# Kernel tuning notes

Measured on AMD Instinct MI355X. Metric: run time of the kernel, lower is better.

Reference implementation:

```python
import jax, jax.numpy as jnp
from jax import lax
import numpy as np

THRESHOLD = 0.8
SECONDARY = 0.6
SECONDARY_WEIGHT = 0.5
BN_EPS = 1e-5


def _conv_relu_pool(x, W, b):
    # x: [B,C,H,W], W: [O,I,3,3]
    y = lax.conv_general_dilated(x, W, window_strides=(1, 1), padding='SAME',
                                 dimension_numbers=('NCHW', 'OIHW', 'NCHW'))
    y = y + b[None, :, None, None]
    y = jax.nn.relu(y)
    return lax.reduce_window(y, -jnp.inf, lax.max, (1, 1, 2, 2), (1, 1, 2, 2), 'VALID')


def setup_inputs() -> dict:
    key = jax.random.key(0)
    ks = jax.random.split(key, 12)
    B, H, W = 1024, 64, 64
    d0, d1, d2 = 4096, 1024, 256  # qnn_arch
    inp = {}
    inp['x'] = jax.random.normal(ks[0], (B, 1, H, W), dtype=jnp.float32)
    # conv params (kaiming-ish scaling)
    inp['cw1'] = jax.random.normal(ks[1], (8, 1, 3, 3), jnp.float32) * (1.0 / np.sqrt(1 * 9))
    inp['cb1'] = jax.random.normal(ks[2], (8,), jnp.float32) * 0.01
    inp['cw2'] = jax.random.normal(ks[3], (16, 8, 3, 3), jnp.float32) * (1.0 / np.sqrt(8 * 9))
    inp['cb2'] = jax.random.normal(ks[4], (16,), jnp.float32) * 0.01
    # linear layers of the 'graph QNN'
    inp['w1'] = jax.random.normal(ks[5], (d1, d0), jnp.float32) * (1.0 / np.sqrt(d0))
    inp['b1'] = jax.random.normal(ks[6], (d1,), jnp.float32) * 0.01
    inp['w2'] = jax.random.normal(ks[7], (d2, d1), jnp.float32) * (1.0 / np.sqrt(d1))
    inp['b2'] = jax.random.normal(ks[8], (d2,), jnp.float32) * 0.01
    # BatchNorm1d affine params
    inp['gamma'] = jnp.ones((d2,), jnp.float32)
    inp['beta'] = jnp.zeros((d2,), jnp.float32)
    return inp


def reference(x, cw1, cb1, cw2, cb2, w1, b1, w2, b2, gamma, beta):
    B = x.shape[0]
    # CNN feature extractor
    feat = _conv_relu_pool(x, cw1, cb1)
    feat = _conv_relu_pool(feat, cw2, cb2)
    flat = feat.reshape(B, -1)                      # [B, 4096]
    # graph-QNN layers with tanh
    h1 = jnp.tanh(flat @ w1.T + b1)                 # [B, 1024]
    last = jnp.tanh(h1 @ w2.T + b2)                 # [B, 256]
    # fidelity adjacency: vectorized normalize + Gram + squared cosine
    norms = jnp.linalg.norm(last, axis=1, keepdims=True)  # [B,1]
    nrm = last / (norms + 1e-12)
    fid = (nrm @ nrm.T) ** 2                        # [B, B]
    adj = jnp.where(fid >= THRESHOLD, 1.0,
                    jnp.where(fid >= SECONDARY, SECONDARY_WEIGHT, 0.0))
    adj = adj * (1.0 - jnp.eye(B, dtype=adj.dtype))  # no self-edges
    # BatchNorm1d (training mode: batch statistics, biased variance)
    mean = jnp.mean(last, axis=0)
    var = jnp.mean((last - mean) ** 2, axis=0)
    out = (last - mean) / jnp.sqrt(var + BN_EPS) * gamma + beta
    return out, adj
```

## Files before the change

kernel.cpp:

```cpp
#include <hip/hip_runtime.h>
#include <hip/hip_bf16.h>
#include <math.h>


__global__ __launch_bounds__(256) void conv1_kernel(
    const float* __restrict__ x, const float* __restrict__ cw1,
    const float* __restrict__ cb1, float* __restrict__ feat1) {
  __shared__ float sX[66 * 66];
  __shared__ float sW1[72];
  __shared__ float sB1[8];

  const int b = blockIdx.x;
  const int t = threadIdx.x;

  for (int i = t; i < 66 * 66; i += 256) sX[i] = 0.0f;
  if (t < 72) sW1[t] = cw1[t];
  if (t < 8)  sB1[t] = cb1[t];
  __syncthreads();

  const float* xb = x + (size_t)b * 4096;
  for (int i = t; i < 4096; i += 256)
    sX[((i >> 6) + 1) * 66 + (i & 63) + 1] = xb[i];
  __syncthreads();

  for (int task = t; task < 2048; task += 256) {
    const int ch = task >> 8;
    const int rem = task & 255;
    const int py = rem >> 3;
    const int px0 = (rem & 7) * 4;

    double w9[9];
#pragma unroll
    for (int k = 0; k < 9; ++k) w9[k] = (double)sW1[ch * 9 + k];

    float reg[4][10];
#pragma unroll
    for (int r = 0; r < 4; ++r)
#pragma unroll
      for (int c = 0; c < 5; ++c) {
        const float2 v =
            *(const float2*)&sX[(2 * py + r) * 66 + 2 * px0 + 2 * c];
        reg[r][2 * c] = v.x;
        reg[r][2 * c + 1] = v.y;
      }

    float out4[4];
#pragma unroll
    for (int px = 0; px < 4; ++px) {
      double best = -1e300;
#pragma unroll
      for (int dy = 0; dy < 2; ++dy) {
#pragma unroll
        for (int dx = 0; dx < 2; ++dx) {
          double s = 0.0;
#pragma unroll
          for (int ky = 0; ky < 3; ++ky)
#pragma unroll
            for (int kx = 0; kx < 3; ++kx)
              s = fma((double)reg[dy + ky][2 * px + dx + kx], w9[ky * 3 + kx],
                      s);
          best = fmax(best, s);
        }
      }
      out4[px] = (float)fmax(best + (double)sB1[ch], 0.0);
    }
    *(float4*)&feat1[(size_t)b * 8192 + ch * 1024 + py * 32 + px0] =
        make_float4(out4[0], out4[1], out4[2], out4[3]);
  }
}

__global__ __launch_bounds__(256) void conv2_kernel(
    const float* __restrict__ feat1, const float* __restrict__ cw2,
    const float* __restrict__ cb2, float* __restrict__ flat) {
  __shared__ float sF[8 * 34 * 34];
  __shared__ float sW2[1152];
  __shared__ float sB2[16];

  const int b = blockIdx.x;
  const int t = threadIdx.x;

  for (int i = t; i < 8 * 34 * 34; i += 256) sF[i] = 0.0f;
  for (int i = t; i < 1152; i += 256) sW2[i] = cw2[i];
  if (t < 16) sB2[t] = cb2[t];
  __syncthreads();

  const float* fb = feat1 + (size_t)b * 8192;
  for (int i = t; i < 8192; i += 256) {
    const int ch = i >> 10, pos = i & 1023;
    sF[ch * 1156 + ((pos >> 5) + 1) * 34 + (pos & 31) + 1] = fb[i];
  }
  __syncthreads();

  const int py = t >> 4, px = t & 15;
  float* ob = flat + (size_t)b * 4096 + py * 16 + px;

#pragma unroll 1
  for (int oh = 0; oh < 2; ++oh) {
    double acc[8][4];
#pragma unroll
    for (int o = 0; o < 8; ++o)
#pragma unroll
      for (int q = 0; q < 4; ++q) acc[o][q] = 0.0;

#pragma unroll
    for (int ic = 0; ic < 8; ++ic) {
      float r[4][4];
#pragma unroll
      for (int iy = 0; iy < 4; ++iy) {
        const float2 v0 =
            *(const float2*)&sF[ic * 1156 + (2 * py + iy) * 34 + 2 * px];
        const float2 v1 =
            *(const float2*)&sF[ic * 1156 + (2 * py + iy) * 34 + 2 * px + 2];
        r[iy][0] = v0.x; r[iy][1] = v0.y; r[iy][2] = v1.x; r[iy][3] = v1.y;
      }
#pragma unroll
      for (int o = 0; o < 8; ++o) {
        const float* w = &sW2[(oh * 8 + o) * 72 + ic * 9];
        double w9[9];
#pragma unroll
        for (int k = 0; k < 9; ++k) w9[k] = (double)w[k];
#pragma unroll
        for (int dy = 0; dy < 2; ++dy)
#pragma unroll
          for (int dx = 0; dx < 2; ++dx) {
            double s = acc[o][dy * 2 + dx];
#pragma unroll
            for (int ky = 0; ky < 3; ++ky)
#pragma unroll
              for (int kx = 0; kx < 3; ++kx)
                s = fma((double)r[dy + ky][dx + kx], w9[ky * 3 + kx], s);
            acc[o][dy * 2 + dx] = s;
          }
      }
    }
#pragma unroll
    for (int o = 0; o < 8; ++o) {
      const int oc = oh * 8 + o;
      const double best =
          fmax(fmax(acc[o][0], acc[o][1]), fmax(acc[o][2], acc[o][3]));
      ob[oc * 256] = (float)fmax(best + (double)sB2[oc], 0.0);
    }
  }
}

__global__ __launch_bounds__(256) void conv_fused(
    const float* __restrict__ x,
    const float* __restrict__ cw1, const float* __restrict__ cb1,
    const float* __restrict__ cw2, const float* __restrict__ cb2,
    float* __restrict__ flat) {
  __shared__ float sX[66 * 66];
  __shared__ float sF[8 * 34 * 34];
  __shared__ float sW1[72];
  __shared__ float sW2[1152];
  __shared__ float sB1[8];
  __shared__ float sB2[16];

  const int b = blockIdx.x;
  const int t = threadIdx.x;

  for (int i = t; i < 66 * 66; i += 256) sX[i] = 0.0f;
  for (int i = t; i < 8 * 34 * 34; i += 256) sF[i] = 0.0f;
  if (t < 72) sW1[t] = cw1[t];
  for (int i = t; i < 1152; i += 256) sW2[i] = cw2[i];
  if (t < 8)  sB1[t] = cb1[t];
  if (t < 16) sB2[t] = cb2[t];
  __syncthreads();

  const float* xb = x + (size_t)b * 4096;
  for (int i = t; i < 4096; i += 256)
    sX[((i >> 6) + 1) * 66 + (i & 63) + 1] = xb[i];
  __syncthreads();

  for (int p = t; p < 8192; p += 256) {
    const int ch = p >> 10, pos = p & 1023;
    const int py1 = pos >> 5, px1 = pos & 31;
    double best = -1e300;
#pragma unroll
    for (int dy = 0; dy < 2; ++dy)
#pragma unroll
      for (int dx = 0; dx < 2; ++dx) {
        const int y = 2 * py1 + dy, xx = 2 * px1 + dx;
        double s = 0.0;
#pragma unroll
        for (int ky = 0; ky < 3; ++ky)
#pragma unroll
          for (int kx = 0; kx < 3; ++kx)
            s = fma((double)sX[(y + ky) * 66 + xx + kx],
                    (double)sW1[ch * 9 + ky * 3 + kx], s);
        best = fmax(best, s);
      }
    sF[ch * 1156 + (py1 + 1) * 34 + px1 + 1] =
        (float)fmax(best + (double)sB1[ch], 0.0);
  }
  __syncthreads();

  const int py = t >> 4, px = t & 15;
  for (int oh = 0; oh < 2; ++oh) {
    double acc[8][4];
#pragma unroll
    for (int o = 0; o < 8; ++o)
#pragma unroll
      for (int q = 0; q < 4; ++q) acc[o][q] = 0.0;
#pragma unroll
    for (int ic = 0; ic < 8; ++ic) {
      double r[4][4];
#pragma unroll
      for (int iy = 0; iy < 4; ++iy)
#pragma unroll
        for (int ix = 0; ix < 4; ++ix)
          r[iy][ix] = (double)sF[ic * 1156 + (2 * py + iy) * 34 + 2 * px + ix];
#pragma unroll
      for (int o = 0; o < 8; ++o) {
        const float* w = &sW2[(oh * 8 + o) * 72 + ic * 9];
        double w9[9];
#pragma unroll
        for (int k = 0; k < 9; ++k) w9[k] = (double)w[k];
#pragma unroll
        for (int dy = 0; dy < 2; ++dy)
#pragma unroll
          for (int dx = 0; dx < 2; ++dx) {
            double s = acc[o][dy * 2 + dx];
#pragma unroll
            for (int ky = 0; ky < 3; ++ky)
#pragma unroll
              for (int kx = 0; kx < 3; ++kx)
                s = fma(r[dy + ky][dx + kx], w9[ky * 3 + kx], s);
            acc[o][dy * 2 + dx] = s;
          }
      }
    }
    float* ob = flat + (size_t)b * 4096 + py * 16 + px;
#pragma unroll
    for (int o = 0; o < 8; ++o) {
      const int oc = oh * 8 + o;
      double best =
          fmax(fmax(acc[o][0], acc[o][1]), fmax(acc[o][2], acc[o][3]));
      ob[oc * 256] = (float)fmax(best + (double)sB2[oc], 0.0);
    }
  }
}

__global__ __launch_bounds__(256) void gemm_nt_f64_v3(
    const float* __restrict__ A, const float* __restrict__ B,
    double* __restrict__ P, int M, int N, int K, int Kc) {
  __shared__ double As[16][130];
  __shared__ double Bs[16][130];

  const int t = threadIdx.x;
  const int n0 = blockIdx.x * 128;
  const int m0 = blockIdx.y * 128;
  const int s  = blockIdx.z;
  const int kb = s * Kc;
  const int rS = t >> 2;
  const int cS = (t & 3) * 4;
  const int ty = t >> 4;
  const int tx = t & 15;

  double acc[8][8];
#pragma unroll
  for (int i = 0; i < 8; ++i)
#pragma unroll
    for (int j = 0; j < 8; ++j) acc[i][j] = 0.0;

  const float* Alo = &A[(size_t)(m0 + rS) * K + cS];
  const float* Ahi = &A[(size_t)(m0 + 64 + rS) * K + cS];
  const float* Blo = &B[(size_t)(n0 + rS) * K + cS];
  const float* Bhi = &B[(size_t)(n0 + 64 + rS) * K + cS];

  float4 a0 = *(const float4*)&Alo[kb];
  float4 a1 = *(const float4*)&Ahi[kb];
  float4 b0 = *(const float4*)&Blo[kb];
  float4 b1 = *(const float4*)&Bhi[kb];

  for (int k0 = kb; k0 < kb + Kc; k0 += 16) {
    __syncthreads();
    As[cS + 0][rS] = (double)a0.x; As[cS + 1][rS] = (double)a0.y;
    As[cS + 2][rS] = (double)a0.z; As[cS + 3][rS] = (double)a0.w;
    As[cS + 0][64 + rS] = (double)a1.x; As[cS + 1][64 + rS] = (double)a1.y;
    As[cS + 2][64 + rS] = (double)a1.z; As[cS + 3][64 + rS] = (double)a1.w;
    Bs[cS + 0][rS] = (double)b0.x; Bs[cS + 1][rS] = (double)b0.y;
    Bs[cS + 2][rS] = (double)b0.z; Bs[cS + 3][rS] = (double)b0.w;
    Bs[cS + 0][64 + rS] = (double)b1.x; Bs[cS + 1][64 + rS] = (double)b1.y;
    Bs[cS + 2][64 + rS] = (double)b1.z; Bs[cS + 3][64 + rS] = (double)b1.w;
    if (k0 + 16 < kb + Kc) {
      a0 = *(const float4*)&Alo[k0 + 16];
      a1 = *(const float4*)&Ahi[k0 + 16];
      b0 = *(const float4*)&Blo[k0 + 16];
      b1 = *(const float4*)&Bhi[k0 + 16];
    }
    __syncthreads();
#pragma unroll
    for (int k = 0; k < 16; ++k) {
      double ar[8], br[8];
#pragma unroll
      for (int g = 0; g < 4; ++g) {
        const double2 av = *(const double2*)&As[k][32 * g + 2 * ty];
        ar[2 * g] = av.x; ar[2 * g + 1] = av.y;
        const double2 bv = *(const double2*)&Bs[k][32 * g + 2 * tx];
        br[2 * g] = bv.x; br[2 * g + 1] = bv.y;
      }
#pragma unroll
      for (int i = 0; i < 8; ++i)
#pragma unroll
        for (int j = 0; j < 8; ++j)
          acc[i][j] = fma(ar[i], br[j], acc[i][j]);
    }
  }

  double* Pp = P + (size_t)s * M * N;
#pragma unroll
  for (int i = 0; i < 8; ++i) {
    const int row = m0 + 32 * (i >> 1) + 2 * ty + (i & 1);
#pragma unroll
    for (int h = 0; h < 4; ++h) {
      const int col = n0 + 32 * h + 2 * tx;
      *(double2*)&Pp[(size_t)row * N + col] =
          make_double2(acc[i][2 * h], acc[i][2 * h + 1]);
    }
  }
}

__global__ __launch_bounds__(256) void reduce_tanh(
    const double* __restrict__ P, int S, const float* __restrict__ bias,
    float* __restrict__ C, int N, int total) {
  const int idx = blockIdx.x * 256 + threadIdx.x;
  if (idx >= total) return;
  double sum = 0.0;
  for (int s = 0; s < S; ++s) sum += P[(size_t)s * total + idx];
  const float zg = (float)sum;
  const float z = zg + bias[idx % N];
  C[idx] = (float)tanh((double)z);
}

__global__ __launch_bounds__(256) void reduce_adj(
    const double* __restrict__ P, int S, float* __restrict__ adj, int N) {
  const int idx = blockIdx.x * 256 + threadIdx.x;
  const int total = N * N;
  if (idx >= total) return;
  double sum = 0.0;
  for (int s = 0; s < S; ++s) sum += P[(size_t)s * total + idx];
  const float g = (float)sum;
  const float fid = g * g;
  float v = (fid >= 0.8f) ? 1.0f : ((fid >= 0.6f) ? 0.5f : 0.0f);
  if (idx / N == idx % N) v = 0.0f;
  adj[idx] = v;
}

__global__ __launch_bounds__(256) void rownorm(
    const float* __restrict__ last, float* __restrict__ nrm) {
  const int b = blockIdx.x;
  const int t = threadIdx.x;
  const float v = last[(size_t)b * 256 + t];
  const float sq = v * v;
  double s = (double)sq;
#pragma unroll
  for (int o = 32; o > 0; o >>= 1) s += __shfl_down(s, o);
  __shared__ double red[4];
  if ((t & 63) == 0) red[t >> 6] = s;
  __syncthreads();
  const double total = red[0] + red[1] + red[2] + red[3];
  const float s32 = (float)total;
  const float den = sqrtf(s32) + 1e-12f;
  nrm[(size_t)b * 256 + t] = v / den;
}

__global__ __launch_bounds__(256) void bn_stats(
    const float* __restrict__ last, const float* __restrict__ gamma,
    const float* __restrict__ beta, float* __restrict__ out) {
  const int j = blockIdx.x;
  const int t = threadIdx.x;
  double v[4];
  double s = 0.0;
#pragma unroll
  for (int i = 0; i < 4; ++i) {
    v[i] = (double)last[(size_t)(i * 256 + t) * 256 + j];
    s += v[i];
  }
#pragma unroll
  for (int o = 32; o > 0; o >>= 1) s += __shfl_down(s, o);
  __shared__ double red[4];
  if ((t & 63) == 0) red[t >> 6] = s;
  __syncthreads();
  const double mean = (red[0] + red[1] + red[2] + red[3]) * (1.0 / 1024.0);
  double q = 0.0;
#pragma unroll
  for (int i = 0; i < 4; ++i) {
    const double d = v[i] - mean;
    q += d * d;
  }
#pragma unroll
  for (int o = 32; o > 0; o >>= 1) q += __shfl_down(q, o);
  __syncthreads();
  if ((t & 63) == 0) red[t >> 6] = q;
  __syncthreads();
  const double var = (red[0] + red[1] + red[2] + red[3]) * (1.0 / 1024.0);
  const double g = (double)gamma[j] / sqrt(var + 1e-5);
  const double be = (double)beta[j];
#pragma unroll
  for (int i = 0; i < 4; ++i)
    out[(size_t)(i * 256 + t) * 256 + j] = (float)((v[i] - mean) * g + be);
}

extern "C" void kernel_launch(void* const* d_in, const int* in_sizes, int n_in,
                              void* d_out, int out_size, void* d_ws,
                              size_t ws_size, hipStream_t stream) {
  const float* x     = (const float*)d_in[0];
  const float* cw1   = (const float*)d_in[1];
  const float* cb1   = (const float*)d_in[2];
  const float* cw2   = (const float*)d_in[3];
  const float* cb2   = (const float*)d_in[4];
  const float* w1    = (const float*)d_in[5];
  const float* b1    = (const float*)d_in[6];
  const float* w2    = (const float*)d_in[7];
  const float* b2    = (const float*)d_in[8];
  const float* gamma = (const float*)d_in[9];
  const float* beta  = (const float*)d_in[10];

  float* outp = (float*)d_out;
  float* adj  = outp + 1024 * 256;

  float* ws   = (float*)d_ws;
  float* flat = ws;
  float* h1   = ws + 4194304;
  float* last = ws + 5242880;
  float* nrm  = ws + 5505024;
  double* part = (double*)(ws + 5767168);
  float* feat1 = (float*)part;

  const size_t baseB = 5767168ull * 4ull;
  int S1;
  if (ws_size >= baseB + 8ull * 1024 * 1024 * 8) S1 = 8;
  else if (ws_size >= baseB + 4ull * 1024 * 1024 * 8) S1 = 4;
  else S1 = 2;
  const int S2 = (S1 >= 4) ? 16 : 4;
  const int S3 = (S1 == 8) ? 4 : 2;
  const bool split_conv = (S1 >= 4);

  if (split_conv) {
    conv1_kernel<<<1024, 256, 0, stream>>>(x, cw1, cb1, feat1);
    conv2_kernel<<<1024, 256, 0, stream>>>(feat1, cw2, cb2, flat);
  } else {
    conv_fused<<<1024, 256, 0, stream>>>(x, cw1, cb1, cw2, cb2, flat);
  }

  gemm_nt_f64_v3<<<dim3(8, 8, S1), 256, 0, stream>>>(
      flat, w1, part, 1024, 1024, 4096, 4096 / S1);
  reduce_tanh<<<4096, 256, 0, stream>>>(part, S1, b1, h1, 1024, 1024 * 1024);

  gemm_nt_f64_v3<<<dim3(2, 8, S2), 256, 0, stream>>>(
      h1, w2, part, 1024, 256, 1024, 1024 / S2);
  reduce_tanh<<<1024, 256, 0, stream>>>(part, S2, b2, last, 256, 1024 * 256);

  rownorm<<<1024, 256, 0, stream>>>(last, nrm);

  gemm_nt_f64_v3<<<dim3(8, 8, S3), 256, 0, stream>>>(
      nrm, nrm, part, 1024, 1024, 256, 256 / S3);
  reduce_adj<<<4096, 256, 0, stream>>>(part, S3, adj, 1024);

  bn_stats<<<256, 256, 0, stream>>>(last, gamma, beta, outp);
}
```

Baseline: 428.8 us.

## Fuse tanh with row norm and compute Gram adjacency directly without split-K

Merges the second reduce_tanh with the row-normalisation kernel so `last` is not re-read from memory. It also replaces the split-K Gram GEMM plus reduce_adj with a single 64x64-tiled fp64 kernel that applies the threshold epilogue in registers, removing the partial-sum buffer traffic and two launches. It additionally allows a deeper split-K (16) for the first GEMM when the workspace is large enough. The direct Gram kernel uses 256 blocks with no K split, which may underfill the GPU compared with the split version.

```diff
diff --git a/kernel.cpp b/kernel.cpp
--- a/kernel.cpp
+++ b/kernel.cpp
@@ -332,25 +332,20 @@
   C[idx] = (float)tanh((double)z);
 }
 
-__global__ __launch_bounds__(256) void reduce_adj(
-    const double* __restrict__ P, int S, float* __restrict__ adj, int N) {
-  const int idx = blockIdx.x * 256 + threadIdx.x;
-  const int total = N * N;
-  if (idx >= total) return;
+__global__ __launch_bounds__(256) void reduce_tanh_norm(
+    const double* __restrict__ P, int S, const float* __restrict__ bias,
+    float* __restrict__ last, float* __restrict__ nrm) {
+  const int b = blockIdx.x;
+  const int t = threadIdx.x;
+  const int idx = b * 256 + t;
+  const int total = 1024 * 256;
   double sum = 0.0;
   for (int s = 0; s < S; ++s) sum += P[(size_t)s * total + idx];
-  const float g = (float)sum;
-  const float fid = g * g;
-  float v = (fid >= 0.8f) ? 1.0f : ((fid >= 0.6f) ? 0.5f : 0.0f);
-  if (idx / N == idx % N) v = 0.0f;
-  adj[idx] = v;
-}
-
-__global__ __launch_bounds__(256) void rownorm(
-    const float* __restrict__ last, float* __restrict__ nrm) {
-  const int b = blockIdx.x;
-  const int t = threadIdx.x;
-  const float v = last[(size_t)b * 256 + t];
+  const float zg = (float)sum;
+  const float z = zg + bias[t];
+  const float v = (float)tanh((double)z);
+  last[idx] = v;
+
   const float sq = v * v;
   double s = (double)sq;
 #pragma unroll
@@ -358,10 +353,70 @@
   __shared__ double red[4];
   if ((t & 63) == 0) red[t >> 6] = s;
   __syncthreads();
-  const double total = red[0] + red[1] + red[2] + red[3];
-  const float s32 = (float)total;
+  const double totalSq = red[0] + red[1] + red[2] + red[3];
+  const float s32 = (float)totalSq;
   const float den = sqrtf(s32) + 1e-12f;
-  nrm[(size_t)b * 256 + t] = v / den;
+  nrm[idx] = v / den;
+}
+
+__global__ __launch_bounds__(256) void gram_adj_direct(
+    const float* __restrict__ Nrm, float* __restrict__ adj, int Msz, int K) {
+  __shared__ double As[16][66];
+  __shared__ double Bs[16][66];
+
+  const int t = threadIdx.x;
+  const int n0 = blockIdx.x * 64;
+  const int m0 = blockIdx.y * 64;
+  const int lm = t >> 2;
+  const int lk4 = (t & 3) * 4;
+  const int ty = t >> 4;
+  const int tx = t & 15;
+
+  double acc[4][4];
+#pragma unroll
+  for (int i = 0; i < 4; ++i)
+#pragma unroll
+    for (int j = 0; j < 4; ++j) acc[i][j] = 0.0;
+
+  for (int k0 = 0; k0 < K; k0 += 16) {
+    const float4 av = *(const float4*)&Nrm[(size_t)(m0 + lm) * K + k0 + lk4];
+    const float4 bv = *(const float4*)&Nrm[(size_t)(n0 + lm) * K + k0 + lk4];
+    __syncthreads();
+    As[lk4 + 0][lm] = (double)av.x; As[lk4 + 1][lm] = (double)av.y;
+    As[lk4 + 2][lm] = (double)av.z; As[lk4 + 3][lm] = (double)av.w;
+    Bs[lk4 + 0][lm] = (double)bv.x; Bs[lk4 + 1][lm] = (double)bv.y;
+    Bs[lk4 + 2][lm] = (double)bv.z; Bs[lk4 + 3][lm] = (double)bv.w;
+    __syncthreads();
+#pragma unroll
+    for (int k = 0; k < 16; ++k) {
+      const double2 a01 = *(const double2*)&As[k][2 * ty];
+      const double2 a23 = *(const double2*)&As[k][32 + 2 * ty];
+      const double2 b01 = *(const double2*)&Bs[k][2 * tx];
+      const double2 b23 = *(const double2*)&Bs[k][32 + 2 * tx];
+      const double ar[4] = {a01.x, a01.y, a23.x, a23.y};
+      const double br[4] = {b01.x, b01.y, b23.x, b23.y};
+#pragma unroll
+      for (int i = 0; i < 4; ++i)
+#pragma unroll
+        for (int j = 0; j < 4; ++j)
+          acc[i][j] = fma(ar[i], br[j], acc[i][j]);
+    }
+  }
+
+  const int rows[4] = {m0 + 2 * ty, m0 + 2 * ty + 1,
+                       m0 + 32 + 2 * ty, m0 + 32 + 2 * ty + 1};
+  const int cols[4] = {n0 + 2 * tx, n0 + 2 * tx + 1,
+                       n0 + 32 + 2 * tx, n0 + 32 + 2 * tx + 1};
+#pragma unroll
+  for (int i = 0; i < 4; ++i)
+#pragma unroll
+    for (int j = 0; j < 4; ++j) {
+      const float g = (float)acc[i][j];
+      const float fid = g * g;
+      float v = (fid >= 0.8f) ? 1.0f : ((fid >= 0.6f) ? 0.5f : 0.0f);
+      if (rows[i] == cols[j]) v = 0.0f;
+      adj[(size_t)rows[i] * Msz + cols[j]] = v;
+    }
 }
 
 __global__ __launch_bounds__(256) void bn_stats(
@@ -429,11 +484,11 @@
 
   const size_t baseB = 5767168ull * 4ull;
   int S1;
-  if (ws_size >= baseB + 8ull * 1024 * 1024 * 8) S1 = 8;
+  if (ws_size >= baseB + 16ull * 1024 * 1024 * 8) S1 = 16;
+  else if (ws_size >= baseB + 8ull * 1024 * 1024 * 8) S1 = 8;
   else if (ws_size >= baseB + 4ull * 1024 * 1024 * 8) S1 = 4;
   else S1 = 2;
   const int S2 = (S1 >= 4) ? 16 : 4;
-  const int S3 = (S1 == 8) ? 4 : 2;
   const bool split_conv = (S1 >= 4);
 
   if (split_conv) {
@@ -449,13 +504,9 @@
 
   gemm_nt_f64_v3<<<dim3(2, 8, S2), 256, 0, stream>>>(
       h1, w2, part, 1024, 256, 1024, 1024 / S2);
-  reduce_tanh<<<1024, 256, 0, stream>>>(part, S2, b2, last, 256, 1024 * 256);
-
-  rownorm<<<1024, 256, 0, stream>>>(last, nrm);
-
-  gemm_nt_f64_v3<<<dim3(8, 8, S3), 256, 0, stream>>>(
-      nrm, nrm, part, 1024, 1024, 256, 256 / S3);
-  reduce_adj<<<4096, 256, 0, stream>>>(part, S3, adj, 1024);
+  reduce_tanh_norm<<<1024, 256, 0, stream>>>(part, S2, b2, last, nrm);
+
+  gram_adj_direct<<<dim3(16, 16), 256, 0, stream>>>(nrm, adj, 1024, 256);
 
   bn_stats<<<256, 256, 0, stream>>>(last, gamma, beta, outp);
 }
```

New measurement: 426.7 us. No clear change (-0.5%).
